# Kernel tuning notes

Hardware: AMD Instinct MI355X
Metric: run time of the kernel (lower is better)

## Reference

```python
import jax, jax.numpy as jnp
import numpy as np

B, IN, OUT, E = 4096, 256, 256, 16


def setup_inputs() -> dict:
    key = jax.random.key(0)
    k1, k2, k3, k4, k5, k6 = jax.random.split(key, 6)
    return {
        "input": jax.random.normal(k1, (B, IN), dtype=jnp.float32),
        "route_index": jax.random.randint(k2, (B,), 0, E),
        "weight": jax.random.normal(k3, (E, OUT * IN), dtype=jnp.float32) * 0.02,
        "weight_fact": jax.random.normal(k4, (1, OUT * IN), dtype=jnp.float32) * 0.02,
        "bias": jax.random.normal(k5, (E, OUT), dtype=jnp.float32) * 0.02,
        "bias_fact": jax.random.normal(k6, (1, OUT), dtype=jnp.float32) * 0.02,
    }


def reference(input, route_index, weight, weight_fact, bias, bias_fact):
    b = input.shape[0]
    # per-token expert weight gather + shared factorized weight
    expert_weight = (weight[route_index] + weight_fact).reshape(b, OUT, IN)
    expert_bias = bias[route_index] + bias_fact  # [b, OUT]
    # batched matvec
    out = jnp.einsum("bmn,bn->bm", expert_weight, input) + expert_bias
    return out
```

## Files before the change

### kernel.cpp

```cpp
#include <hip/hip_runtime.h>


#define B_TOK 4096
#define IN_F 256
#define OUT_F 256
#define NEXP 16
#define WEL (OUT_F * IN_F)
#define MAX_TILES (B_TOK / 16 + NEXP)

typedef __attribute__((ext_vector_type(8))) short bhalf8;
typedef __attribute__((ext_vector_type(4))) float v4f;

#define WSUM_OFF 0u
#define XBF_OFF 2097152u
#define BSUM_OFF 4194304u
#define STOK_OFF 4210688u
#define PART_OFF 4227072u
#define META_OFF 4228096u
#define DESC_OFF 4228352u

__device__ __forceinline__ unsigned short f2bf(float f) {
    unsigned u = __float_as_uint(f);
    u += 0x7FFFu + ((u >> 16) & 1u);
    return (unsigned short)(u >> 16);
}

__global__ __launch_bounds__(256) void k_prep(
    const float* __restrict__ x, const int* __restrict__ ridx,
    const float* __restrict__ w, const float* __restrict__ wf,
    const float* __restrict__ bias, const float* __restrict__ bf,
    unsigned short* __restrict__ wsum, unsigned short* __restrict__ xbf,
    float* __restrict__ bsum, int* __restrict__ part) {
    int bid = blockIdx.x;
    int tid = threadIdx.x;
    if (bid < 512) {
        int id = (bid * 256 + tid) * 8;
        const float4 a0 = *(const float4*)(w + id);
        const float4 a1 = *(const float4*)(w + id + 4);
        int fo = id & (WEL - 1);
        const float4 f0 = *(const float4*)(wf + fo);
        const float4 f1 = *(const float4*)(wf + fo + 4);
        bhalf8 v;
        v[0] = (short)f2bf(a0.x + f0.x); v[1] = (short)f2bf(a0.y + f0.y);
        v[2] = (short)f2bf(a0.z + f0.z); v[3] = (short)f2bf(a0.w + f0.w);
        v[4] = (short)f2bf(a1.x + f1.x); v[5] = (short)f2bf(a1.y + f1.y);
        v[6] = (short)f2bf(a1.z + f1.z); v[7] = (short)f2bf(a1.w + f1.w);
        *(bhalf8*)(wsum + id) = v;
    } else if (bid < 1024) {
        int id = ((bid - 512) * 256 + tid) * 8;
        const float4 a0 = *(const float4*)(x + id);
        const float4 a1 = *(const float4*)(x + id + 4);
        bhalf8 v;
        v[0] = (short)f2bf(a0.x); v[1] = (short)f2bf(a0.y);
        v[2] = (short)f2bf(a0.z); v[3] = (short)f2bf(a0.w);
        v[4] = (short)f2bf(a1.x); v[5] = (short)f2bf(a1.y);
        v[6] = (short)f2bf(a1.z); v[7] = (short)f2bf(a1.w);
        *(bhalf8*)(xbf + id) = v;
    } else if (bid < 1028) {
        int id = ((bid - 1024) * 256 + tid) * 4;
        const float4 a = *(const float4*)(bias + id);
        const float4 f = *(const float4*)(bf + (id & (OUT_F - 1)));
        float4 r;
        r.x = a.x + f.x; r.y = a.y + f.y; r.z = a.z + f.z; r.w = a.w + f.w;
        *(float4*)(bsum + id) = r;
    } else {
        __shared__ int h[NEXP];
        if (tid < NEXP) h[tid] = 0;
        __syncthreads();
        int hb = bid - 1028;
        atomicAdd(&h[ridx[hb * 256 + tid]], 1);
        __syncthreads();
        if (tid < NEXP) part[hb * NEXP + tid] = h[tid];
    }
}

__global__ __launch_bounds__(256) void k_plan(const int* __restrict__ part,
                                              int* __restrict__ meta,
                                              int* __restrict__ desc) {
    __shared__ int counts[NEXP];
    __shared__ int base[NEXP];
    __shared__ int tbase[NEXP + 1];
    int t = threadIdx.x;
    if (t < NEXP) {
        int c = 0;
        for (int b = 0; b < 16; ++b) c += part[b * NEXP + t];
        counts[t] = c;
    }
    __syncthreads();
    if (t == 0) {
        int acc = 0, tb = 0;
        for (int e = 0; e < NEXP; ++e) {
            base[e] = acc;
            tbase[e] = tb;
            meta[e] = acc;
            meta[16 + e] = acc;
            acc += counts[e];
            tb += (counts[e] + 15) >> 4;
        }
        tbase[NEXP] = tb;
        meta[32] = tb;
    }
    __syncthreads();
    int nt = tbase[NEXP];
    for (int i = t; i < MAX_TILES; i += 256) {
        if (i < nt) {
            int e = 0;
            while (!(i >= tbase[e] && i < tbase[e + 1])) ++e;
            int j = i - tbase[e];
            int rem = counts[e] - j * 16;
            desc[i * 3 + 0] = e;
            desc[i * 3 + 1] = base[e] + j * 16;
            desc[i * 3 + 2] = rem < 16 ? rem : 16;
        }
    }
}

__global__ __launch_bounds__(256) void k_scatter(const int* __restrict__ ridx,
                                                 int* __restrict__ meta,
                                                 int* __restrict__ stok) {
    __shared__ int lc[NEXP];
    __shared__ int gb[NEXP];
    int t = threadIdx.x;
    if (t < NEXP) lc[t] = 0;
    __syncthreads();
    int tok = blockIdx.x * 256 + t;
    int e = ridx[tok];
    int r = atomicAdd(&lc[e], 1);
    __syncthreads();
    if (t < NEXP) gb[t] = atomicAdd(&meta[16 + t], lc[t]);
    __syncthreads();
    stok[gb[e] + r] = tok;
}

__global__ __launch_bounds__(256) void k_gemm(
    const unsigned short* __restrict__ wsum, const unsigned short* __restrict__ xbf,
    const float* __restrict__ bsum, const int* __restrict__ stok,
    const int* __restrict__ meta, const int* __restrict__ desc,
    float* __restrict__ out) {
    int nt_total = meta[32];
    int t = blockIdx.x;
    if (t >= nt_total) return;
    int e = desc[t * 3 + 0];
    int start = desc[t * 3 + 1];
    int rows = desc[t * 3 + 2];

    __shared__ int stk[16];
    int tid = threadIdx.x;
    if (tid < 16) {
        int i = tid < rows ? tid : rows - 1;
        stk[tid] = stok[start + i];
    }
    __syncthreads();

    int lane = tid & 63;
    int wave = tid >> 6;
    int l15 = lane & 15;
    int quad = lane >> 4;

    const unsigned short* xrow = xbf + stk[l15] * IN_F + quad * 8;
    const unsigned short* wbase =
        wsum + e * WEL + (wave * 64 + l15) * IN_F + quad * 8;

    v4f acc[4];
    #pragma unroll
    for (int n = 0; n < 4; ++n) acc[n] = (v4f){0.f, 0.f, 0.f, 0.f};

    #pragma unroll
    for (int ks = 0; ks < 8; ++ks) {
        bhalf8 a = *(const bhalf8*)(xrow + ks * 32);
        bhalf8 b0 = *(const bhalf8*)(wbase + 0 * 16 * IN_F + ks * 32);
        bhalf8 b1 = *(const bhalf8*)(wbase + 1 * 16 * IN_F + ks * 32);
        bhalf8 b2 = *(const bhalf8*)(wbase + 2 * 16 * IN_F + ks * 32);
        bhalf8 b3 = *(const bhalf8*)(wbase + 3 * 16 * IN_F + ks * 32);
        acc[0] = __builtin_amdgcn_mfma_f32_16x16x32_bf16(a, b0, acc[0], 0, 0, 0);
        acc[1] = __builtin_amdgcn_mfma_f32_16x16x32_bf16(a, b1, acc[1], 0, 0, 0);
        acc[2] = __builtin_amdgcn_mfma_f32_16x16x32_bf16(a, b2, acc[2], 0, 0, 0);
        acc[3] = __builtin_amdgcn_mfma_f32_16x16x32_bf16(a, b3, acc[3], 0, 0, 0);
    }

    #pragma unroll
    for (int n = 0; n < 4; ++n) {
        int m = wave * 64 + n * 16 + l15;
        float bb = bsum[e * OUT_F + m];
        #pragma unroll
        for (int r = 0; r < 4; ++r) {
            int row = quad * 4 + r;
            if (row < rows) out[stk[row] * OUT_F + m] = acc[n][r] + bb;
        }
    }
}

extern "C" void kernel_launch(void* const* d_in, const int* in_sizes, int n_in,
                              void* d_out, int out_size, void* d_ws, size_t ws_size,
                              hipStream_t stream) {
    const float* x = (const float*)d_in[0];
    const int* ridx = (const int*)d_in[1];
    const float* w = (const float*)d_in[2];
    const float* wf = (const float*)d_in[3];
    const float* bias = (const float*)d_in[4];
    const float* bf = (const float*)d_in[5];
    float* out = (float*)d_out;
    char* ws = (char*)d_ws;

    unsigned short* wsum = (unsigned short*)(ws + WSUM_OFF);
    unsigned short* xbf = (unsigned short*)(ws + XBF_OFF);
    float* bsum = (float*)(ws + BSUM_OFF);
    int* stok = (int*)(ws + STOK_OFF);
    int* part = (int*)(ws + PART_OFF);
    int* meta = (int*)(ws + META_OFF);
    int* desc = (int*)(ws + DESC_OFF);

    k_prep<<<1044, 256, 0, stream>>>(x, ridx, w, wf, bias, bf, wsum, xbf, bsum, part);
    k_plan<<<1, 256, 0, stream>>>(part, meta, desc);
    k_scatter<<<16, 256, 0, stream>>>(ridx, meta, stok);
    k_gemm<<<MAX_TILES, 256, 0, stream>>>(wsum, xbf, bsum, stok, meta, desc, out);
}
```

Measured before the change: 88.97 us.

## Merge plan and scatter kernels, index GEMM tiles by expert grid

```diff
diff --git a/kernel.cpp b/kernel.cpp
--- a/kernel.cpp
+++ b/kernel.cpp
@@ -6,7 +6,6 @@
 #define OUT_F 256
 #define NEXP 16
 #define WEL (OUT_F * IN_F)
-#define MAX_TILES (B_TOK / 16 + NEXP)
 
 typedef __attribute__((ext_vector_type(8))) short bhalf8;
 typedef __attribute__((ext_vector_type(4))) float v4f;
@@ -17,7 +16,6 @@
 #define STOK_OFF 4210688u
 #define PART_OFF 4227072u
 #define META_OFF 4228096u
-#define DESC_OFF 4228352u
 
 __device__ __forceinline__ unsigned short f2bf(float f) {
     unsigned u = __float_as_uint(f);
@@ -74,75 +72,57 @@
     }
 }
 
-__global__ __launch_bounds__(256) void k_plan(const int* __restrict__ part,
-                                              int* __restrict__ meta,
-                                              int* __restrict__ desc) {
-    __shared__ int counts[NEXP];
+__global__ __launch_bounds__(256) void k_scatplan(
+    const int* __restrict__ part, const int* __restrict__ ridx,
+    int* __restrict__ meta, int* __restrict__ stok) {
+    __shared__ int pl[256];
+    __shared__ int tot[NEXP];
     __shared__ int base[NEXP];
-    __shared__ int tbase[NEXP + 1];
+    __shared__ int boff[NEXP];
+    __shared__ int lrank[NEXP];
     int t = threadIdx.x;
+    int b = blockIdx.x;
+    pl[t] = part[t];
+    if (t < NEXP) lrank[t] = 0;
+    __syncthreads();
     if (t < NEXP) {
-        int c = 0;
-        for (int b = 0; b < 16; ++b) c += part[b * NEXP + t];
-        counts[t] = c;
+        int s = 0, o = 0;
+        for (int bb = 0; bb < 16; ++bb) {
+            int v = pl[bb * NEXP + t];
+            s += v;
+            if (bb < b) o += v;
+        }
+        tot[t] = s;
+        boff[t] = o;
     }
     __syncthreads();
-    if (t == 0) {
-        int acc = 0, tb = 0;
-        for (int e = 0; e < NEXP; ++e) {
-            base[e] = acc;
-            tbase[e] = tb;
-            meta[e] = acc;
-            meta[16 + e] = acc;
-            acc += counts[e];
-            tb += (counts[e] + 15) >> 4;
+    if (t < NEXP) {
+        int a = 0;
+        for (int ee = 0; ee < t; ++ee) a += tot[ee];
+        base[t] = a;
+        if (b == 0) {
+            meta[t] = a;
+            meta[NEXP + t] = tot[t];
         }
-        tbase[NEXP] = tb;
-        meta[32] = tb;
     }
     __syncthreads();
-    int nt = tbase[NEXP];
-    for (int i = t; i < MAX_TILES; i += 256) {
-        if (i < nt) {
-            int e = 0;
-            while (!(i >= tbase[e] && i < tbase[e + 1])) ++e;
-            int j = i - tbase[e];
-            int rem = counts[e] - j * 16;
-            desc[i * 3 + 0] = e;
-            desc[i * 3 + 1] = base[e] + j * 16;
-            desc[i * 3 + 2] = rem < 16 ? rem : 16;
-        }
-    }
-}
-
-__global__ __launch_bounds__(256) void k_scatter(const int* __restrict__ ridx,
-                                                 int* __restrict__ meta,
-                                                 int* __restrict__ stok) {
-    __shared__ int lc[NEXP];
-    __shared__ int gb[NEXP];
-    int t = threadIdx.x;
-    if (t < NEXP) lc[t] = 0;
-    __syncthreads();
-    int tok = blockIdx.x * 256 + t;
+    int tok = b * 256 + t;
     int e = ridx[tok];
-    int r = atomicAdd(&lc[e], 1);
-    __syncthreads();
-    if (t < NEXP) gb[t] = atomicAdd(&meta[16 + t], lc[t]);
-    __syncthreads();
-    stok[gb[e] + r] = tok;
+    int r = atomicAdd(&lrank[e], 1);
+    stok[base[e] + boff[e] + r] = tok;
 }
 
 __global__ __launch_bounds__(256) void k_gemm(
     const unsigned short* __restrict__ wsum, const unsigned short* __restrict__ xbf,
     const float* __restrict__ bsum, const int* __restrict__ stok,
-    const int* __restrict__ meta, const int* __restrict__ desc,
-    float* __restrict__ out) {
-    int nt_total = meta[32];
-    int t = blockIdx.x;
-    if (t >= nt_total) return;
-    int e = desc[t * 3 + 0];
-    int start = desc[t * 3 + 1];
-    int rows = desc[t * 3 + 2];
+    const int* __restrict__ meta, float* __restrict__ out) {
+    int e = blockIdx.y;
+    int cnt = meta[NEXP + e];
+    int j16 = blockIdx.x * 16;
+    if (j16 >= cnt) return;
+    int start = meta[e] + j16;
+    int rem = cnt - j16;
+    int rows = rem < 16 ? rem : 16;
 
     __shared__ int stk[16];
     int tid = threadIdx.x;
@@ -208,10 +188,8 @@
     int* stok = (int*)(ws + STOK_OFF);
     int* part = (int*)(ws + PART_OFF);
     int* meta = (int*)(ws + META_OFF);
-    int* desc = (int*)(ws + DESC_OFF);
 
     k_prep<<<1044, 256, 0, stream>>>(x, ridx, w, wf, bias, bf, wsum, xbf, bsum, part);
-    k_plan<<<1, 256, 0, stream>>>(part, meta, desc);
-    k_scatter<<<16, 256, 0, stream>>>(ridx, meta, stok);
-    k_gemm<<<MAX_TILES, 256, 0, stream>>>(wsum, xbf, bsum, stok, meta, desc, out);
+    k_scatplan<<<16, 256, 0, stream>>>(part, ridx, meta, stok);
+    k_gemm<<<dim3(256, NEXP), 256, 0, stream>>>(wsum, xbf, bsum, stok, meta, out);
 }
```

Result: slower. 107.2 us (+20.5%).
